# Kernel optimization log

Hardware: AMD Instinct MI355X
Metric: run time of the kernel (lower is better)

Reference implementation:

```python
import jax, jax.numpy as jnp
import numpy as np

RADIUS = 0.1
K = 32  # num_neighbors


def setup_inputs() -> dict:
    key = jax.random.key(0)
    k1, k2, k3 = jax.random.split(key, 3)
    B, N, M, C = 4, 16384, 4096, 64
    points_coords = jax.random.uniform(k1, (B, 3, N), dtype=jnp.float32)
    centers_coords = jax.random.uniform(k2, (B, 3, M), dtype=jnp.float32)
    points_features = jax.random.normal(k3, (B, C, N), dtype=jnp.float32)
    return {
        "points_coords": points_coords,
        "centers_coords": centers_coords,
        "points_features": points_features,
    }


def _ball_query_indices(points_coords, centers_coords, radius, k):
    """Return [B, M, K] int32 indices of up to k points within radius of each
    center; slots beyond the in-ball count are padded with the first in-ball
    index (0 if the ball is empty), matching PVCNN's ball_query semantics."""
    B, _, N = points_coords.shape
    # squared pairwise distances [B, M, N]
    p2 = jnp.sum(points_coords * points_coords, axis=1)          # [B, N]
    c2 = jnp.sum(centers_coords * centers_coords, axis=1)        # [B, M]
    cp = jnp.einsum('bdm,bdn->bmn', centers_coords, points_coords)
    d2 = c2[:, :, None] + p2[None if False else slice(None), None, :] - 2.0 * cp
    valid = d2 < (radius * radius)
    # candidate index if in ball, else sentinel N; first k in index order
    cand = jnp.where(valid, jnp.arange(N, dtype=jnp.int32)[None, None, :],
                     jnp.int32(N))
    topk = -jax.lax.top_k(-cand, k)[0]                           # ascending
    first = topk[..., :1]
    idx = jnp.where(topk == N, first, topk)   # pad with first in-ball index
    idx = jnp.where(idx == N, 0, idx)         # empty ball -> index 0
    return idx


def _group(feat, idx):
    # feat: [B, C, N], idx: [B, M, K] -> [B, C, M, K]
    return jax.vmap(lambda f, i: f[:, i])(feat, idx)


def reference(points_coords, centers_coords, points_features):
    idx = _ball_query_indices(points_coords, centers_coords, RADIUS, K)
    idx = jax.lax.stop_gradient(idx)
    # relative neighbor coordinates [B, 3, M, K]
    neighbor_coords = _group(points_coords, idx) - centers_coords[:, :, :, None]
    neighbor_features = _group(points_features, idx)             # [B, C, M, K]
    return jnp.concatenate([neighbor_coords, neighbor_features], axis=1)
```

## Files before the change

kernel.cpp:

```cpp
#include <hip/hip_runtime.h>
#include <climits>

#define KNN 32
#define NPTS 16384
#define MCTR 4096
#define BATCH 4
#define CFEAT 64
#define NBINS 1000
#define HITCAP 128
#define CPW 4
#define WCHUNKS 8
#define FPAD 34

typedef float f4 __attribute__((ext_vector_type(4)));

__device__ __forceinline__ bool ball_pred(float cx, float cy, float cz, float c2,
                                          float px, float py, float pz) {
    const float r2 = 0.009999999776482582f;
    const float p2 = __fmaf_rn(pz, pz, __fmaf_rn(px, px, __fmul_rn(py, py)));
    const float cp = __fmaf_rn(cz, pz, __fmaf_rn(cy, py, __fmul_rn(cx, px)));
    const float d2 = __fsub_rn(__fadd_rn(c2, p2), __fmul_rn(2.0f, cp));
    return d2 < r2;
}

__device__ __forceinline__ int bin_of(float x, float y, float z) {
    int bx = min(max((int)(x * 10.0f), 0), 9);
    int by = min(max((int)(y * 10.0f), 0), 9);
    int bz = min(max((int)(z * 10.0f), 0), 9);
    return (bx * 10 + by) * 10 + bz;
}

__global__ __launch_bounds__(256) void bin_count(const float* __restrict__ points,
                                                 int* __restrict__ counts) {
    const int t = blockIdx.x * 256 + threadIdx.x;
    const int b = t >> 14, i = t & (NPTS - 1);
    const float* pc = points + (size_t)b * 3 * NPTS;
    atomicAdd(&counts[b * NBINS + bin_of(pc[i], pc[NPTS + i], pc[2 * NPTS + i])], 1);
}

__global__ __launch_bounds__(256) void bin_scan(const int* __restrict__ counts,
                                                int* __restrict__ binStart,
                                                int* __restrict__ cursor) {
    __shared__ int sm[256];
    const int b = blockIdx.x, t = threadIdx.x;
    int c[4];
    int ls = 0;
#pragma unroll
    for (int i = 0; i < 4; ++i) {
        const int bin = t * 4 + i;
        c[i] = (bin < NBINS) ? counts[b * NBINS + bin] : 0;
        ls += c[i];
    }
    sm[t] = ls;
    __syncthreads();
    for (int off = 1; off < 256; off <<= 1) {
        int v = (t >= off) ? sm[t - off] : 0;
        __syncthreads();
        sm[t] += v;
        __syncthreads();
    }
    int run = sm[t] - ls;
#pragma unroll
    for (int i = 0; i < 4; ++i) {
        const int bin = t * 4 + i;
        if (bin < NBINS) {
            binStart[b * (NBINS + 1) + bin] = run;
            cursor[b * NBINS + bin] = run;
        }
        run += c[i];
    }
    if (t == 255) binStart[b * (NBINS + 1) + NBINS] = sm[255];
}

__global__ __launch_bounds__(256) void bin_scatter(const float* __restrict__ points,
                                                   int* __restrict__ cursor,
                                                   f4* __restrict__ sP,
                                                   f4* __restrict__ pointsT) {
    const int t = blockIdx.x * 256 + threadIdx.x;
    const int b = t >> 14, i = t & (NPTS - 1);
    const float* pc = points + (size_t)b * 3 * NPTS;
    const float x = pc[i], y = pc[NPTS + i], z = pc[2 * NPTS + i];
    pointsT[(size_t)b * NPTS + i] = (f4){x, y, z, 0.0f};
    const int pos = atomicAdd(&cursor[b * NBINS + bin_of(x, y, z)], 1);
    sP[(size_t)b * NPTS + pos] = (f4){x, y, z, __int_as_float(i)};
}

__global__ __launch_bounds__(256) void transpose_kernel(
    const float* __restrict__ feats, float* __restrict__ featsT)
{
    __shared__ float tl[64][65];
    const int b  = blockIdx.x >> 8;
    const int n0 = (blockIdx.x & 255) * 64;
    const float* f = feats  + (size_t)b * CFEAT * NPTS;
    float* ft      = featsT + (size_t)b * NPTS * CFEAT;
    const int t = threadIdx.x;
    const int nl = t & 63, cq = t >> 6;
#pragma unroll
    for (int r = 0; r < 16; ++r) {
        const int ch = r * 4 + cq;
        tl[ch][nl] = __builtin_nontemporal_load(&f[(size_t)ch * NPTS + n0 + nl]);
    }
    __syncthreads();
    const int chl = t & 63, nq = t >> 6;
#pragma unroll
    for (int r = 0; r < 16; ++r) {
        const int n = r * 4 + nq;
        ft[(size_t)(n0 + n) * CFEAT + chl] = tl[chl][n];
    }
}

__global__ __launch_bounds__(64) void bq_gather_fused(
    const float* __restrict__ points, const float* __restrict__ centers,
    const int* __restrict__ binStart, const f4* __restrict__ sP,
    const f4* __restrict__ pointsT, const float* __restrict__ featsT,
    float* __restrict__ out)
{
    __shared__ int hits[HITCAP];
    __shared__ float lfeat[KNN][FPAD];
    const int lane = threadIdx.x;
    const int cls = blockIdx.x & 7;
    const int b   = cls >> 1;
    const int m   = ((cls & 1) << 11) | (blockIdx.x >> 3);

    const float* cc = centers + (size_t)b * 3 * MCTR;
    const float cx = cc[m], cy = cc[MCTR + m], cz = cc[2 * MCTR + m];
    const float c2 = __fmaf_rn(cz, cz, __fmaf_rn(cx, cx, __fmul_rn(cy, cy)));

    hits[lane] = INT_MAX;
    hits[lane + 64] = INT_MAX;

    const float rg = 0.1001f;
    const int xlo = max((int)((cx - rg) * 10.0f), 0), xhi = min((int)((cx + rg) * 10.0f), 9);
    const int ylo = max((int)((cy - rg) * 10.0f), 0), yhi = min((int)((cy + rg) * 10.0f), 9);
    const int zlo = max((int)((cz - rg) * 10.0f), 0), zhi = min((int)((cz + rg) * 10.0f), 9);

    const int base = b * NPTS;
    const int* bs = binStart + b * (NBINS + 1);
    int cnt = 0;

    for (int X = xlo; X <= xhi; ++X) {
        for (int Y = ylo; Y <= yhi; ++Y) {
            const int cb = (X * 10 + Y) * 10;
            const int s = bs[cb + zlo];
            const int e = bs[cb + zhi + 1];
            for (int p = s; p < e; p += 64) {
                const int o = p + lane;
                const bool in = o < e;
                const f4 P = in ? sP[base + o] : (f4){1e9f, 1e9f, 1e9f, 0.0f};
                const bool valid = in && ball_pred(cx, cy, cz, c2, P.x, P.y, P.z);
                const unsigned long long mask = __ballot(valid);
                if (mask) {
                    const int prefix = __popcll(mask & ((1ull << lane) - 1ull));
                    const int ppos = cnt + prefix;
                    if (valid && ppos < HITCAP) hits[ppos] = __float_as_int(P.w);
                    cnt += __popcll(mask);
                }
            }
        }
    }

    int fidx;
    if (cnt > HITCAP) {
        const float* pc = points + (size_t)b * 3 * NPTS;
        int cnt2 = 0, firstIdx = 0;
        for (int j0 = 0; j0 < NPTS; j0 += 64) {
            const int j = j0 + lane;
            const bool valid = ball_pred(cx, cy, cz, c2, pc[j], pc[NPTS + j], pc[2 * NPTS + j]);
            const unsigned long long mask = __ballot(valid);
            if (mask) {
                if (cnt2 == 0) firstIdx = j0 + __builtin_ctzll(mask);
                const int prefix = __popcll(mask & ((1ull << lane) - 1ull));
                if (valid && (cnt2 + prefix) < KNN) hits[cnt2 + prefix] = j;
                cnt2 += __popcll(mask);
                if (cnt2 >= KNN) break;
            }
        }
        const int first = (cnt2 == 0) ? 0 : firstIdx;
        fidx = (lane < cnt2 && lane < KNN) ? hits[lane] : first;
    } else {
        int a  = hits[lane];
        int v2 = hits[lane + 64];
#pragma unroll
        for (int k = 2; k <= 128; k <<= 1) {
#pragma unroll
            for (int j = 64; j >= 1; j >>= 1) {
                if (j > (k >> 1)) continue;
                if (j == 64) {
                    const int lo = min(a, v2), hi = max(a, v2);
                    a = lo; v2 = hi;
                } else {
                    const bool lower = (lane & j) == 0;
                    const bool upA = (lane & k) == 0;
                    const bool upB = ((lane + 64) & k) == 0;
                    const int va = __shfl_xor(a, j);
                    a = (lower == upA) ? min(a, va) : max(a, va);
                    const int vb = __shfl_xor(v2, j);
                    v2 = (lower == upB) ? min(v2, vb) : max(v2, vb);
                }
            }
        }
        const int first = __shfl(a, 0);
        fidx = (lane < cnt) ? a : ((cnt == 0) ? 0 : first);
    }

    float* obase = out + ((size_t)b * 67 * MCTR + m) * KNN;

    if (lane < 32) {
        const f4 P = pointsT[(size_t)base + fidx];
        obase[lane]                          = P.x - cx;
        obase[(size_t)MCTR * KNN + lane]     = P.y - cy;
        obase[(size_t)2 * MCTR * KNN + lane] = P.z - cz;
    }

    const float* ft = featsT + (size_t)b * NPTS * CFEAT;
    const int pp = lane >> 3;
    const int q  = lane & 7;
    const int ch8 = lane >> 3;
    const int kq  = lane & 7;
#pragma unroll
    for (int h = 0; h < 2; ++h) {
#pragma unroll
        for (int s = 0; s < 4; ++s) {
            const int k = s * 8 + pp;
            const int ik = __shfl(fidx, k);
            const float4 v = *reinterpret_cast<const float4*>(
                ft + (size_t)ik * CFEAT + h * 32 + q * 4);
            *reinterpret_cast<float2*>(&lfeat[k][4 * q])     = make_float2(v.x, v.y);
            *reinterpret_cast<float2*>(&lfeat[k][4 * q + 2]) = make_float2(v.z, v.w);
        }
#pragma unroll
        for (int it = 0; it < 4; ++it) {
            const int cw = it * 8 + ch8;
            const int ch = h * 32 + cw;
            float4 o;
            o.x = lfeat[4 * kq + 0][cw];
            o.y = lfeat[4 * kq + 1][cw];
            o.z = lfeat[4 * kq + 2][cw];
            o.w = lfeat[4 * kq + 3][cw];
            *reinterpret_cast<float4*>(&obase[(size_t)(3 + ch) * MCTR * KNN + 4 * kq]) = o;
        }
    }
}

__global__ __launch_bounds__(256) void ball_query_kernel(
    const float* __restrict__ points, const float* __restrict__ centers,
    int* __restrict__ idx_out)
{
    const int wave = (blockIdx.x * blockDim.x + threadIdx.x) >> 6;
    const int lane = threadIdx.x & 63;
    const int wavesPerBatch = MCTR / CPW;
    const int b = wave / wavesPerBatch;
    const int m0 = (wave % wavesPerBatch) * CPW;

    const float* pc = points + (size_t)b * 3 * NPTS;
    const float* cc = centers + (size_t)b * 3 * MCTR;

    float cx[CPW], cy[CPW], cz[CPW], c2[CPW];
    int cnt[CPW], firstIdx[CPW];
#pragma unroll
    for (int c = 0; c < CPW; ++c) {
        cx[c] = cc[m0 + c]; cy[c] = cc[MCTR + m0 + c]; cz[c] = cc[2 * MCTR + m0 + c];
        c2[c] = __fmaf_rn(cz[c], cz[c], __fmaf_rn(cx[c], cx[c], __fmul_rn(cy[c], cy[c])));
        cnt[c] = 0; firstIdx[c] = 0;
    }
    int* outbase = idx_out + ((size_t)b * MCTR + m0) * KNN;

    for (int w = 0; w < NPTS / (64 * WCHUNKS); ++w) {
        const int base = w * 64 * WCHUNKS + lane;
        float px[WCHUNKS], py[WCHUNKS], pz[WCHUNKS];
#pragma unroll
        for (int u = 0; u < WCHUNKS; ++u) {
            px[u] = pc[base + 64 * u];
            py[u] = pc[NPTS + base + 64 * u];
            pz[u] = pc[2 * NPTS + base + 64 * u];
        }
#pragma unroll
        for (int u = 0; u < WCHUNKS; ++u) {
            const int j0 = w * 64 * WCHUNKS + 64 * u;
            const int j = j0 + lane;
#pragma unroll
            for (int c = 0; c < CPW; ++c) {
                const bool valid = ball_pred(cx[c], cy[c], cz[c], c2[c], px[u], py[u], pz[u]);
                const unsigned long long mask = __ballot(valid);
                if (mask) {
                    if (cnt[c] == 0) firstIdx[c] = j0 + __builtin_ctzll(mask);
                    const int prefix = __popcll(mask & ((1ull << lane) - 1ull));
                    if (valid && (cnt[c] + prefix) < KNN)
                        outbase[c * KNN + cnt[c] + prefix] = j;
                    cnt[c] += __popcll(mask);
                }
            }
        }
        bool alldone = true;
#pragma unroll
        for (int c = 0; c < CPW; ++c) alldone &= (cnt[c] >= KNN);
        if (alldone) break;
    }
#pragma unroll
    for (int c = 0; c < CPW; ++c) {
        if (cnt[c] < KNN && lane >= cnt[c] && lane < KNN)
            outbase[c * KNN + lane] = firstIdx[c];
    }
}

__global__ __launch_bounds__(256) void gather_direct_kernel(
    const float* __restrict__ points, const float* __restrict__ centers,
    const float* __restrict__ feats, const int* __restrict__ idx,
    float* __restrict__ out)
{
    const long long t = (long long)blockIdx.x * blockDim.x + threadIdx.x;
    const int k = (int)(t & (KNN - 1));
    long long r = t >> 5;
    const int m = (int)(r & (MCTR - 1));
    r >>= 12;
    const int ch = (int)(r % 67);
    const int b = (int)(r / 67);
    const int i = idx[((size_t)(b * MCTR + m)) * KNN + k];
    float v;
    if (ch < 3) {
        v = points[(size_t)b * 3 * NPTS + (size_t)ch * NPTS + i]
          - centers[(size_t)b * 3 * MCTR + (size_t)ch * MCTR + m];
    } else {
        v = feats[(size_t)b * CFEAT * NPTS + (size_t)(ch - 3) * NPTS + i];
    }
    out[t] = v;
}

extern "C" void kernel_launch(void* const* d_in, const int* in_sizes, int n_in,
                              void* d_out, int out_size, void* d_ws, size_t ws_size,
                              hipStream_t stream) {
    const float* points  = nullptr;
    const float* centers = nullptr;
    const float* feats   = nullptr;
    for (int i = 0; i < n_in; ++i) {
        if (in_sizes[i] == BATCH * 3 * NPTS)      points  = (const float*)d_in[i];
        else if (in_sizes[i] == BATCH * 3 * MCTR) centers = (const float*)d_in[i];
        else if (in_sizes[i] == BATCH * CFEAT * NPTS) feats = (const float*)d_in[i];
    }
    float* out = (float*)d_out;

    size_t off = 0;
    auto carve = [&](size_t bytes) -> void* {
        void* p = (char*)d_ws + off;
        off = (off + bytes + 255) & ~(size_t)255;
        return p;
    };
    int*   idx      = (int*)  carve((size_t)BATCH * MCTR * KNN * 4);
    float* featsT   = (float*)carve((size_t)BATCH * NPTS * CFEAT * 4);
    int*   counts   = (int*)  carve((size_t)BATCH * NBINS * 4);
    int*   cursor   = (int*)  carve((size_t)BATCH * NBINS * 4);
    int*   binStart = (int*)  carve((size_t)BATCH * (NBINS + 1) * 4);
    f4*    sP       = (f4*)   carve((size_t)BATCH * NPTS * 16);
    f4*    pointsT  = (f4*)   carve((size_t)BATCH * NPTS * 16);
    const size_t neededFull = off;

    if (ws_size >= neededFull) {
        (void)hipMemsetAsync(counts, 0, (size_t)BATCH * NBINS * 4, stream);
        bin_count<<<BATCH * NPTS / 256, 256, 0, stream>>>(points, counts);
        bin_scan<<<BATCH, 256, 0, stream>>>(counts, binStart, cursor);
        bin_scatter<<<BATCH * NPTS / 256, 256, 0, stream>>>(points, cursor, sP, pointsT);
        transpose_kernel<<<BATCH * (NPTS / 64), 256, 0, stream>>>(feats, featsT);
        bq_gather_fused<<<BATCH * MCTR, 64, 0, stream>>>(
            points, centers, binStart, sP, pointsT, featsT, out);
    } else {
        const int nThreads1 = (BATCH * MCTR / CPW) * 64;
        ball_query_kernel<<<nThreads1 / 256, 256, 0, stream>>>(points, centers, idx);
        const long long total = (long long)BATCH * 67 * MCTR * KNN;
        gather_direct_kernel<<<(int)(total / 256), 256, 0, stream>>>(points, centers, feats, idx, out);
    }
}
```

Baseline: 71.81 us.

## Fuse binning count/scan/scatter into one per-batch kernel and vectorize transpose stores

Replaces the memset plus three binning kernels (global atomic count, scan, global atomic scatter) with a single 1024-thread block per batch that builds the histogram in shared memory, scans it, and scatters using shared-memory cursors. This removes three launches, a memset and global atomics. The cost is that only four blocks do the binning, so that stage uses very little of the GPU. Separately, the feature transpose now writes float4 vectors instead of scalar stores.

```diff
diff --git a/kernel.cpp b/kernel.cpp
--- a/kernel.cpp
+++ b/kernel.cpp
@@ -30,59 +30,59 @@
     return (bx * 10 + by) * 10 + bz;
 }
 
-__global__ __launch_bounds__(256) void bin_count(const float* __restrict__ points,
-                                                 int* __restrict__ counts) {
-    const int t = blockIdx.x * 256 + threadIdx.x;
-    const int b = t >> 14, i = t & (NPTS - 1);
+__global__ __launch_bounds__(1024) void bin_prep(
+    const float* __restrict__ points,
+    int* __restrict__ binStart,
+    f4* __restrict__ sP,
+    f4* __restrict__ pointsT)
+{
+    __shared__ int hist[NBINS];
+    __shared__ int scanbuf[1024];
+    const int b = blockIdx.x;
+    const int t = threadIdx.x;
     const float* pc = points + (size_t)b * 3 * NPTS;
-    atomicAdd(&counts[b * NBINS + bin_of(pc[i], pc[NPTS + i], pc[2 * NPTS + i])], 1);
-}
-
-__global__ __launch_bounds__(256) void bin_scan(const int* __restrict__ counts,
-                                                int* __restrict__ binStart,
-                                                int* __restrict__ cursor) {
-    __shared__ int sm[256];
-    const int b = blockIdx.x, t = threadIdx.x;
-    int c[4];
-    int ls = 0;
-#pragma unroll
-    for (int i = 0; i < 4; ++i) {
-        const int bin = t * 4 + i;
-        c[i] = (bin < NBINS) ? counts[b * NBINS + bin] : 0;
-        ls += c[i];
-    }
-    sm[t] = ls;
-    __syncthreads();
-    for (int off = 1; off < 256; off <<= 1) {
-        int v = (t >= off) ? sm[t - off] : 0;
+    const size_t gb = (size_t)b * NPTS;
+
+    if (t < NBINS) hist[t] = 0;
+    __syncthreads();
+
+    f4 myp[16];
+    int mybin[16];
+#pragma unroll
+    for (int r = 0; r < 16; ++r) {
+        const int i = r * 1024 + t;
+        const float x = pc[i], y = pc[NPTS + i], z = pc[2 * NPTS + i];
+        myp[r] = (f4){x, y, z, __int_as_float(i)};
+        pointsT[gb + i] = (f4){x, y, z, 0.0f};
+        const int bn = bin_of(x, y, z);
+        mybin[r] = bn;
+        atomicAdd(&hist[bn], 1);
+    }
+    __syncthreads();
+
+    const int v = (t < NBINS) ? hist[t] : 0;
+    scanbuf[t] = v;
+    __syncthreads();
+    for (int off = 1; off < 1024; off <<= 1) {
+        const int u = (t >= off) ? scanbuf[t - off] : 0;
         __syncthreads();
-        sm[t] += v;
+        scanbuf[t] += u;
         __syncthreads();
     }
-    int run = sm[t] - ls;
-#pragma unroll
-    for (int i = 0; i < 4; ++i) {
-        const int bin = t * 4 + i;
-        if (bin < NBINS) {
-            binStart[b * (NBINS + 1) + bin] = run;
-            cursor[b * NBINS + bin] = run;
-        }
-        run += c[i];
-    }
-    if (t == 255) binStart[b * (NBINS + 1) + NBINS] = sm[255];
-}
-
-__global__ __launch_bounds__(256) void bin_scatter(const float* __restrict__ points,
-                                                   int* __restrict__ cursor,
-                                                   f4* __restrict__ sP,
-                                                   f4* __restrict__ pointsT) {
-    const int t = blockIdx.x * 256 + threadIdx.x;
-    const int b = t >> 14, i = t & (NPTS - 1);
-    const float* pc = points + (size_t)b * 3 * NPTS;
-    const float x = pc[i], y = pc[NPTS + i], z = pc[2 * NPTS + i];
-    pointsT[(size_t)b * NPTS + i] = (f4){x, y, z, 0.0f};
-    const int pos = atomicAdd(&cursor[b * NBINS + bin_of(x, y, z)], 1);
-    sP[(size_t)b * NPTS + pos] = (f4){x, y, z, __int_as_float(i)};
+    const int excl = scanbuf[t] - v;
+    if (t < NBINS) {
+        binStart[b * (NBINS + 1) + t] = excl;
+    }
+    if (t == 0) binStart[b * (NBINS + 1) + NBINS] = NPTS;
+    __syncthreads();
+    if (t < NBINS) hist[t] = excl;
+    __syncthreads();
+
+#pragma unroll
+    for (int r = 0; r < 16; ++r) {
+        const int pos = atomicAdd(&hist[mybin[r]], 1);
+        sP[gb + pos] = myp[r];
+    }
 }
 
 __global__ __launch_bounds__(256) void transpose_kernel(
@@ -101,11 +101,17 @@
         tl[ch][nl] = __builtin_nontemporal_load(&f[(size_t)ch * NPTS + n0 + nl]);
     }
     __syncthreads();
-    const int chl = t & 63, nq = t >> 6;
-#pragma unroll
-    for (int r = 0; r < 16; ++r) {
-        const int n = r * 4 + nq;
-        ft[(size_t)(n0 + n) * CFEAT + chl] = tl[chl][n];
+    const int quad = t & 15;
+    const int ngrp = t >> 4;
+#pragma unroll
+    for (int r = 0; r < 4; ++r) {
+        const int n = r * 16 + ngrp;
+        f4 o;
+        o.x = tl[4 * quad + 0][n];
+        o.y = tl[4 * quad + 1][n];
+        o.z = tl[4 * quad + 2][n];
+        o.w = tl[4 * quad + 3][n];
+        *reinterpret_cast<f4*>(&ft[(size_t)(n0 + n) * CFEAT + 4 * quad]) = o;
     }
 }
 
@@ -347,18 +353,13 @@
     };
     int*   idx      = (int*)  carve((size_t)BATCH * MCTR * KNN * 4);
     float* featsT   = (float*)carve((size_t)BATCH * NPTS * CFEAT * 4);
-    int*   counts   = (int*)  carve((size_t)BATCH * NBINS * 4);
-    int*   cursor   = (int*)  carve((size_t)BATCH * NBINS * 4);
     int*   binStart = (int*)  carve((size_t)BATCH * (NBINS + 1) * 4);
     f4*    sP       = (f4*)   carve((size_t)BATCH * NPTS * 16);
     f4*    pointsT  = (f4*)   carve((size_t)BATCH * NPTS * 16);
     const size_t neededFull = off;
 
     if (ws_size >= neededFull) {
-        (void)hipMemsetAsync(counts, 0, (size_t)BATCH * NBINS * 4, stream);
-        bin_count<<<BATCH * NPTS / 256, 256, 0, stream>>>(points, counts);
-        bin_scan<<<BATCH, 256, 0, stream>>>(counts, binStart, cursor);
-        bin_scatter<<<BATCH * NPTS / 256, 256, 0, stream>>>(points, cursor, sP, pointsT);
+        bin_prep<<<BATCH, 1024, 0, stream>>>(points, binStart, sP, pointsT);
         transpose_kernel<<<BATCH * (NPTS / 64), 256, 0, stream>>>(feats, featsT);
         bq_gather_fused<<<BATCH * MCTR, 64, 0, stream>>>(
             points, centers, binStart, sP, pointsT, featsT, out);
```

Measured after the change: 70.30 us. 1.02x faster.
